# Performance work log

Measured on AMD Instinct MI355X. Metric: run time of the kernel, lower is better.

The kernel has to match this reference:

```python
import jax, jax.numpy as jnp
import numpy as np

N = 100000   # nodes
E = 1600000  # edges per relation
R = 3        # relations
F = 128      # feature_size
H = 64       # hid_dim
O = 32       # out_dim
B = 50000    # batch_nodes
EPS = 1e-5


def setup_inputs() -> dict:
    key = jax.random.key(0)
    ks = jax.random.split(key, 14)
    inp = {
        "features": jax.random.normal(ks[0], (N, F), jnp.float32),
        "edge_index": jax.random.randint(ks[1], (R, 2, E), 0, N),
        "batch_nodes": jax.random.randint(ks[2], (B,), 0, N),
        # per-relation conv1 / conv2 weights
        "W1": jax.random.normal(ks[3], (R, F, H), jnp.float32) / np.sqrt(F),
        "b1": jnp.zeros((R, H), jnp.float32),
        "W2": jax.random.normal(ks[4], (R, H, O), jnp.float32) / np.sqrt(H),
        "b2": jnp.zeros((R, O), jnp.float32),
        # learnable gamma (init 0.5) per conv per relation
        "gamma1": jnp.full((R,), 0.5, jnp.float32),
        "gamma2": jnp.full((R,), 0.5, jnp.float32),
        # batchnorm affine params per relation
        "bn1_scale": jnp.ones((R, H), jnp.float32),
        "bn1_bias": jnp.zeros((R, H), jnp.float32),
        "bn2_scale": jnp.ones((R, O), jnp.float32),
        "bn2_bias": jnp.zeros((R, O), jnp.float32),
    }
    return inp


def _pfgcn_conv(x, W, b, src, dst, gamma):
    # linear transform then symmetric-normalized gather/scatter aggregation,
    # mixed with self features via learnable gamma
    h = x @ W + b                                        # [N, C]
    deg = jax.ops.segment_sum(jnp.ones((src.shape[0],), h.dtype), dst, num_segments=N)
    dinv = jax.lax.rsqrt(jnp.maximum(deg, 1.0))          # [N]
    norm = dinv[src] * dinv[dst]                         # [E]
    agg = jax.ops.segment_sum(h[src] * norm[:, None], dst, num_segments=N)
    return gamma * agg + (1.0 - gamma) * h


def _batchnorm(x, scale, bias):
    m = x.mean(axis=0)
    v = x.var(axis=0)
    return (x - m) * jax.lax.rsqrt(v + EPS) * scale + bias


def reference(features, edge_index, batch_nodes, W1, b1, W2, b2,
              gamma1, gamma2, bn1_scale, bn1_bias, bn2_scale, bn2_bias):
    embeds = []
    for r in range(R):  # small fixed relation count
        src, dst = edge_index[r, 0], edge_index[r, 1]
        x = _pfgcn_conv(features, W1[r], b1[r], src, dst, gamma1[r])
        x = jax.nn.relu(_batchnorm(x, bn1_scale[r], bn1_bias[r]))
        # dropout is identity in eval
        x = _pfgcn_conv(x, W2[r], b2[r], src, dst, gamma2[r])
        x = jax.nn.relu(_batchnorm(x, bn2_scale[r], bn2_bias[r]))
        embeds.append(jax.nn.log_softmax(x[batch_nodes], axis=1))  # [B, O]
    multi = jnp.stack(embeds, axis=1)          # [B, R, O]
    return multi.reshape(batch_nodes.shape[0], -1)  # [B, R*O]
```

## Files before the change

### kernel.cpp

```cpp
#include <hip/hip_runtime.h>
#include <hip/hip_fp16.h>
#include <math.h>

#define N_NODES 100000
#define N_PAD   100352
#define N_EDGES 1600000
#define N_REL   3
#define BN_EPS  1e-5f

#define BK    49
#define BSH   11
#define BMSK  2047
#define NBLK  250
#define EPB   6400


__global__ __launch_bounds__(256) void k_hist(const int* __restrict__ ei,
                                              int* __restrict__ offs,
                                              float* __restrict__ zeroRegion) {
    const int r = blockIdx.y;
    const int* dst = ei + (size_t)r * 2 * N_EDGES + N_EDGES;
    const int tid = threadIdx.x;
    if (blockIdx.x == 0 && r == 0) {
        for (int i = tid; i < N_REL * 192; i += 256) zeroRegion[i] = 0.0f;
    }
    __shared__ int hist[4][BK];
    for (int i = tid; i < 4 * BK; i += 256) (&hist[0][0])[i] = 0;
    __syncthreads();
    const int4* d4 = (const int4*)(dst + blockIdx.x * EPB);
    const int cpy = tid & 3;
    for (int i = tid; i < EPB / 4; i += 256) {
        int4 v = d4[i];
        atomicAdd(&hist[cpy][v.x >> BSH], 1);
        atomicAdd(&hist[cpy][v.y >> BSH], 1);
        atomicAdd(&hist[cpy][v.z >> BSH], 1);
        atomicAdd(&hist[cpy][v.w >> BSH], 1);
    }
    __syncthreads();
    if (tid < BK)
        offs[(size_t)r * BK * NBLK + tid * NBLK + blockIdx.x] =
            hist[0][tid] + hist[1][tid] + hist[2][tid] + hist[3][tid];
}

__global__ __launch_bounds__(1024) void k_histscan(int* __restrict__ offs) {
    const int r = blockIdx.x;
    int* o = offs + (size_t)r * BK * NBLK;
    constexpr int LEN = BK * NBLK;
    constexpr int PER = (LEN + 1023) / 1024;
    __shared__ int sh[1024];
    const int t = threadIdx.x;
    const int base = t * PER;
    int pre[PER];
    int lsum = 0;
    #pragma unroll
    for (int i = 0; i < PER; ++i) {
        int idx = base + i;
        int v = (idx < LEN) ? o[idx] : 0;
        pre[i] = lsum;
        lsum += v;
    }
    sh[t] = lsum;
    __syncthreads();
    for (int s = 1; s < 1024; s <<= 1) {
        int add = (t >= s) ? sh[t - s] : 0;
        __syncthreads();
        sh[t] += add;
        __syncthreads();
    }
    const int myoff = sh[t] - lsum;
    #pragma unroll
    for (int i = 0; i < PER; ++i) {
        int idx = base + i;
        if (idx < LEN) o[idx] = myoff + pre[i];
    }
}

__global__ __launch_bounds__(256) void k_bin(const int* __restrict__ ei,
                                             const int* __restrict__ offs,
                                             int* __restrict__ binned) {
    const int r = blockIdx.y;
    const int* src = ei + (size_t)r * 2 * N_EDGES;
    const int* dst = src + N_EDGES;
    int* bn = binned + (size_t)r * N_EDGES;
    const int tid = threadIdx.x;
    __shared__ int cur[BK];
    if (tid < BK)
        cur[tid] = offs[(size_t)r * BK * NBLK + tid * NBLK + blockIdx.x];
    __syncthreads();
    const int4* s4p = (const int4*)(src + blockIdx.x * EPB);
    const int4* d4p = (const int4*)(dst + blockIdx.x * EPB);
    for (int i = tid; i < EPB / 4; i += 256) {
        int4 s4 = s4p[i];
        int4 dd = d4p[i];
        int p0 = atomicAdd(&cur[dd.x >> BSH], 1);
        bn[p0] = s4.x | ((dd.x & BMSK) << 17);
        int p1 = atomicAdd(&cur[dd.y >> BSH], 1);
        bn[p1] = s4.y | ((dd.y & BMSK) << 17);
        int p2 = atomicAdd(&cur[dd.z >> BSH], 1);
        bn[p2] = s4.z | ((dd.z & BMSK) << 17);
        int p3 = atomicAdd(&cur[dd.w >> BSH], 1);
        bn[p3] = s4.w | ((dd.w & BMSK) << 17);
    }
}

__global__ __launch_bounds__(1024) void k_csr2(const int* __restrict__ binned,
                                               const int* __restrict__ offs,
                                               int* __restrict__ rowptr,
                                               float* __restrict__ dinvB,
                                               float* __restrict__ rdinvB,
                                               int* __restrict__ edsrc) {
    const int r = blockIdx.y;
    const int b = blockIdx.x;
    const int t = threadIdx.x;
    const int bbase = b << BSH;
    const int* o = offs + (size_t)r * BK * NBLK;
    const int start = o[b * NBLK];
    const int end = (b == BK - 1) ? N_EDGES : o[(b + 1) * NBLK];
    const int* bn = binned + (size_t)r * N_EDGES;
    int* ed = edsrc + (size_t)r * N_EDGES;
    int* rp = rowptr + (size_t)r * (N_PAD + 1);
    float* dinv  = dinvB  + (size_t)r * N_PAD;
    float* rdinv = rdinvB + (size_t)r * N_PAD;

    __shared__ int cnt[1 << BSH];
    __shared__ int ssum[1024];
    cnt[t] = 0;
    cnt[t + 1024] = 0;
    __syncthreads();
    for (int i = start + t; i < end; i += 1024)
        atomicAdd(&cnt[bn[i] >> 17], 1);
    __syncthreads();
    const int a0 = cnt[2 * t];
    const int a1 = cnt[2 * t + 1];
    const int lsum = a0 + a1;
    ssum[t] = lsum;
    __syncthreads();
    for (int s = 1; s < 1024; s <<= 1) {
        int add = (t >= s) ? ssum[t - s] : 0;
        __syncthreads();
        ssum[t] += add;
        __syncthreads();
    }
    const int ex = ssum[t] - lsum;
    const int p0 = start + ex;
    const int p1 = p0 + a0;
    const int n0g = bbase + 2 * t;
    if (n0g < N_NODES) {
        rp[n0g] = p0;
        float m = fmaxf((float)a0, 1.0f);
        float dv = rsqrtf(m);
        dinv[n0g] = dv;
        rdinv[n0g] = m * dv;
    }
    if (n0g + 1 < N_NODES) {
        rp[n0g + 1] = p1;
        float m = fmaxf((float)a1, 1.0f);
        float dv = rsqrtf(m);
        dinv[n0g + 1] = dv;
        rdinv[n0g + 1] = m * dv;
    }
    if (b == BK - 1 && t == 0) rp[N_NODES] = N_EDGES;
    cnt[2 * t] = p0;
    cnt[2 * t + 1] = p1;
    __syncthreads();
    for (int i = start + t; i < end; i += 1024) {
        int p = bn[i];
        int pos = atomicAdd(&cnt[p >> 17], 1);
        ed[pos] = p & 0x1FFFF;
    }
}

__device__ __forceinline__ float ld_f(const float* p)  { return *p; }
__device__ __forceinline__ float ld_f(const __half* p) { return __half2float(*p); }

template<int K, int C, bool BN, typename TI>
__global__ __launch_bounds__(256) void k_gemm(const TI* __restrict__ Xb,
                                              size_t xStrideR,
                                              const float* __restrict__ Wb,
                                              const float* __restrict__ biasB,
                                              const float* __restrict__ bnsumB,
                                              const float* __restrict__ bnsqB,
                                              const float* __restrict__ bnScaleB,
                                              const float* __restrict__ bnBiasB,
                                              const float* __restrict__ dinvB,
                                              __half* __restrict__ Yb,
                                              int nodesPerBlock) {
    const int r = blockIdx.y;
    const TI* X = Xb + (size_t)r * xStrideR;
    const float* W = Wb + (size_t)r * K * C;
    const float* bias = biasB + (size_t)r * C;
    const float* dinv = dinvB + (size_t)r * N_PAD;
    __half* Y = Yb + (size_t)r * N_NODES * C;

    constexpr int CG = C / 4;
    constexpr int NPASS = 256 / CG;
    constexpr int XP = K + 1;
    __shared__ __align__(16) float Ws[K * C];
    __shared__ float Xs[NPASS * XP];
    __shared__ float seL[K], beL[K];
    const int tid = threadIdx.x;
    for (int i = tid; i < K * C; i += 256) Ws[i] = W[i];
    if (BN) {
        for (int i = tid; i < K; i += 256) {
            int gi = r * K + i;
            float m = bnsumB[gi] * (1.0f / N_NODES);
            float v = bnsqB[gi] * (1.0f / N_NODES) - m * m;
            float inv = rsqrtf(v + BN_EPS);
            float sc = inv * bnScaleB[gi];
            seL[i] = sc;
            beL[i] = bnBiasB[gi] - m * sc;
        }
    }
    const int cg = tid % CG;
    const int ln = tid / CG;
    const int c0 = cg * 4;
    const float4 bv = *(const float4*)&bias[c0];
    const int blockStart = blockIdx.x * nodesPerBlock;
    const int passes = nodesPerBlock / NPASS;
    for (int p = 0; p < passes; ++p) {
        const int node0 = blockStart + p * NPASS;
        __syncthreads();
        for (int i = tid; i < NPASS * K; i += 256) {
            int lnn = i / K, k = i % K;
            int n = node0 + lnn;
            float v = 0.0f;
            if (n < N_NODES) {
                v = ld_f(&X[(size_t)n * K + k]);
                if (BN) v = fmaxf(v * seL[k] + beL[k], 0.0f);
            }
            Xs[lnn * XP + k] = v;
        }
        __syncthreads();
        const int n = node0 + ln;
        float4 acc = bv;
        const float* xrow = &Xs[ln * XP];
        #pragma unroll 8
        for (int k = 0; k < K; ++k) {
            float f = xrow[k];
            float4 w = *(const float4*)&Ws[k * C + c0];
            acc.x += f * w.x;
            acc.y += f * w.y;
            acc.z += f * w.z;
            acc.w += f * w.w;
        }
        if (n < N_NODES) {
            const float dv = dinv[n];
            ushort4 sv;
            sv.x = __half_as_ushort(__float2half_rn(acc.x * dv));
            sv.y = __half_as_ushort(__float2half_rn(acc.y * dv));
            sv.z = __half_as_ushort(__float2half_rn(acc.z * dv));
            sv.w = __half_as_ushort(__float2half_rn(acc.w * dv));
            *(ushort4*)&Y[(size_t)n * C + c0] = sv;
        }
    }
}

template<int C, int NPB, typename TO>
__global__ __launch_bounds__(256) void k_gather(const __half* __restrict__ hB,
                                                const int* __restrict__ rowptrB,
                                                const int* __restrict__ edsB,
                                                const float* __restrict__ dinvB,
                                                const float* __restrict__ rdinvB,
                                                const float* __restrict__ gammaP,
                                                TO* __restrict__ XB,
                                                float* __restrict__ bnsumB,
                                                float* __restrict__ bnsqB) {
    const int r = blockIdx.y;
    const __half* h = hB + (size_t)r * N_NODES * C;
    const int* rowptr = rowptrB + (size_t)r * (N_PAD + 1);
    const int* edg = edsB + (size_t)r * N_EDGES;
    const float* dinv  = dinvB  + (size_t)r * N_PAD;
    const float* rdinv = rdinvB + (size_t)r * N_PAD;
    TO* X = XB + (size_t)r * N_NODES * C;
    float* bnsum = bnsumB + (size_t)r * C;
    float* bnsq  = bnsqB  + (size_t)r * C;

    constexpr int WPB = 256 / C;
    constexpr int RPS = NPB / WPB;
    constexpr int CH  = 4096;
    __shared__ int eds[CH];
    __shared__ int rp[NPB + 1];
    __shared__ float red[256];
    const int tid = threadIdx.x;
    const int c = tid % C;
    const int slot = tid / C;
    const float g = gammaP[r];
    const float gi = 1.0f - g;
    const int n0 = blockIdx.x * NPB;
    const __half* hc = h + c;
    if (tid <= NPB) {
        int n = n0 + tid;
        rp[tid] = rowptr[(n <= N_NODES) ? n : N_NODES];
    }
    __syncthreads();
    const int bs = rp[0];
    const int bEnd = rp[NPB];
    int rs[RPS], re[RPS];
    float acc[RPS];
    #pragma unroll
    for (int i = 0; i < RPS; ++i) {
        int ri = slot + i * WPB;
        rs[i] = rp[ri];
        re[i] = rp[ri + 1];
        acc[i] = 0.0f;
    }
    for (int ck = bs; ck < bEnd; ck += CH) {
        const int c1 = min(ck + CH, bEnd);
        const int cnt = c1 - ck;
        __syncthreads();
        for (int j = tid; j < cnt; j += 256) eds[j] = edg[ck + j];
        __syncthreads();
        #pragma unroll
        for (int i = 0; i < RPS; ++i) {
            const int lo = max(rs[i], ck);
            const int hi = min(re[i], c1);
            if (lo >= hi) continue;
            float a = acc[i];
            int e = lo;
            const int efull = lo + ((hi - lo) & ~7);
            for (; e < efull; e += 8) {
                int ed[8];
                #pragma unroll
                for (int j = 0; j < 8; ++j) ed[j] = eds[e - ck + j];
                float v[8];
                #pragma unroll
                for (int j = 0; j < 8; ++j)
                    v[j] = __half2float(hc[(unsigned)ed[j] * C]);
                #pragma unroll
                for (int j = 0; j < 8; ++j) a += v[j];
            }
            if (e < hi) {
                int ed[8];
                #pragma unroll
                for (int j = 0; j < 8; ++j) {
                    int t = e + j;
                    ed[j] = eds[((t < hi) ? t : lo) - ck];
                }
                float v[8];
                #pragma unroll
                for (int j = 0; j < 8; ++j)
                    v[j] = __half2float(hc[(unsigned)ed[j] * C]);
                #pragma unroll
                for (int j = 0; j < 8; ++j)
                    a += (e + j < hi) ? v[j] : 0.0f;
            }
            acc[i] = a;
        }
    }
    float s = 0.0f, sq = 0.0f;
    #pragma unroll
    for (int i = 0; i < RPS; ++i) {
        int n = n0 + slot + i * WPB;
        if (n < N_NODES) {
            float x = g * dinv[n] * acc[i]
                    + gi * rdinv[n] * __half2float(hc[(unsigned)n * C]);
            if constexpr (sizeof(TO) == 2)
                X[(size_t)n * C + c] = __float2half_rn(x);
            else
                X[(size_t)n * C + c] = x;
            s += x;
            sq += x * x;
        }
    }
    __syncthreads();
    red[tid] = s;
    __syncthreads();
    if (slot == 0) {
        float t = 0.0f;
        #pragma unroll
        for (int i = 0; i < WPB; ++i) t += red[c + i * C];
        atomicAdd(&bnsum[c], t);
    }
    __syncthreads();
    red[tid] = sq;
    __syncthreads();
    if (slot == 0) {
        float t = 0.0f;
        #pragma unroll
        for (int i = 0; i < WPB; ++i) t += red[c + i * C];
        atomicAdd(&bnsq[c], t);
    }
}

__global__ __launch_bounds__(256) void k_out(const float* __restrict__ x2B,
                                             const int* __restrict__ batch,
                                             const float* __restrict__ bnsumB,
                                             const float* __restrict__ bnsqB,
                                             const float* __restrict__ scaleB,
                                             const float* __restrict__ biasB,
                                             float* __restrict__ out) {
    const int r = blockIdx.y;
    const float* x2 = x2B + (size_t)r * N_NODES * 32;
    __shared__ float seL[32], beL[32];
    if (threadIdx.x < 32) {
        int gi = r * 32 + threadIdx.x;
        float m = bnsumB[gi] * (1.0f / N_NODES);
        float v = bnsqB[gi] * (1.0f / N_NODES) - m * m;
        float inv = rsqrtf(v + BN_EPS);
        float sc = inv * scaleB[gi];
        seL[threadIdx.x] = sc;
        beL[threadIdx.x] = biasB[gi] - m * sc;
    }
    __syncthreads();
    int gid = blockIdx.x * 256 + threadIdx.x;
    int b = gid >> 5;
    int c = gid & 31;
    if (b < 50000) {
        int node = batch[b];
        float y = fmaxf(x2[(size_t)node * 32 + c] * seL[c] + beL[c], 0.0f);
        float m = y;
        #pragma unroll
        for (int off = 16; off; off >>= 1) m = fmaxf(m, __shfl_xor(m, off, 32));
        float ex = __expf(y - m);
        float ssum = ex;
        #pragma unroll
        for (int off = 16; off; off >>= 1) ssum += __shfl_xor(ssum, off, 32);
        out[(size_t)b * (N_REL * 32) + r * 32 + c] = (y - m) - __logf(ssum);
    }
}

extern "C" void kernel_launch(void* const* d_in, const int* in_sizes, int n_in,
                              void* d_out, int out_size, void* d_ws, size_t ws_size,
                              hipStream_t stream) {
    const float* features    = (const float*)d_in[0];
    const int*   edge_index  = (const int*)d_in[1];
    const int*   batch_nodes = (const int*)d_in[2];
    const float* W1          = (const float*)d_in[3];
    const float* b1          = (const float*)d_in[4];
    const float* W2          = (const float*)d_in[5];
    const float* b2          = (const float*)d_in[6];
    const float* gamma1      = (const float*)d_in[7];
    const float* gamma2      = (const float*)d_in[8];
    const float* bn1_scale   = (const float*)d_in[9];
    const float* bn1_bias    = (const float*)d_in[10];
    const float* bn2_scale   = (const float*)d_in[11];
    const float* bn2_bias    = (const float*)d_in[12];
    float* out = (float*)d_out;

    char* wsB = (char*)d_ws;
    size_t off = 0;
    auto alloc = [&](size_t bytes) {
        void* p = wsB + off;
        off = (off + bytes + 15) & ~(size_t)15;
        return p;
    };
    float* bnsum1 = (float*)alloc(N_REL * 64 * 4);
    float* bnsq1  = (float*)alloc(N_REL * 64 * 4);
    float* bnsum2 = (float*)alloc(N_REL * 32 * 4);
    float* bnsq2  = (float*)alloc(N_REL * 32 * 4);
    float* zeroRegion = bnsum1;
    float* dinv      = (float*)alloc((size_t)N_REL * N_PAD * 4);
    float* rdinv     = (float*)alloc((size_t)N_REL * N_PAD * 4);
    int*   rowptr    = (int*)alloc((size_t)N_REL * (N_PAD + 1) * 4);
    int*   offs      = (int*)alloc((size_t)N_REL * BK * NBLK * 4);
    int*    edsrc = (int*)alloc((size_t)N_REL * N_EDGES * 4);
    __half* h1   = (__half*)alloc((size_t)N_REL * N_NODES * 64 * 2);
    __half* x1   = (__half*)alloc((size_t)N_REL * N_NODES * 64 * 2);
    __half* h2   = (__half*)alloc((size_t)N_REL * N_NODES * 32 * 2);
    float*  x2   = (float*)h1;
    int*  binned = (int*)x1;

    k_hist<<<dim3(NBLK, N_REL), 256, 0, stream>>>(edge_index, offs, zeroRegion);
    k_histscan<<<N_REL, 1024, 0, stream>>>(offs);
    k_bin<<<dim3(NBLK, N_REL), 256, 0, stream>>>(edge_index, offs, binned);
    k_csr2<<<dim3(BK, N_REL), 1024, 0, stream>>>(binned, offs, rowptr,
                                                 dinv, rdinv, edsrc);

    k_gemm<128, 64, false, float><<<dim3((N_NODES + 63) / 64, N_REL), 256, 0, stream>>>(
        features, 0, W1, b1, nullptr, nullptr, nullptr, nullptr, dinv, h1, 64);
    k_gather<64, 32, __half><<<dim3((N_NODES + 31) / 32, N_REL), 256, 0, stream>>>(
        h1, rowptr, edsrc, dinv, rdinv, gamma1, x1, bnsum1, bnsq1);

    k_gemm<64, 32, true, __half><<<dim3((N_NODES + 127) / 128, N_REL), 256, 0, stream>>>(
        x1, (size_t)N_NODES * 64, W2, b2, bnsum1, bnsq1, bn1_scale, bn1_bias,
        dinv, h2, 128);
    k_gather<32, 64, float><<<dim3((N_NODES + 63) / 64, N_REL), 256, 0, stream>>>(
        h2, rowptr, edsrc, dinv, rdinv, gamma2, x2, bnsum2, bnsq2);

    k_out<<<dim3((50000 * 32 + 255) / 256, N_REL), 256, 0, stream>>>(
        x2, batch_nodes, bnsum2, bnsq2, bn2_scale, bn2_bias, out);
}
```

Baseline: 781.1 us.

## Rewrite CSR gather as warp-per-row with vectorized loads and XCD-aware block mapping

The gather kernel now gives each 64-lane wavefront one destination row at a time. Lanes split into groups that each load four half channels per edge (8-byte vector loads), and edge indices are broadcast by shuffle instead of staged in a shared-memory chunk. Partial sums are reduced across groups with xor shuffles. Blocks are remapped so consecutive work groups of the same relation land on the same XCD, for L2 locality. The shared-memory edge staging and per-channel scalar half loads go away, at the cost of shuffle reductions and possible idle lanes on low-degree rows.

```diff
diff --git a/kernel.cpp b/kernel.cpp
--- a/kernel.cpp
+++ b/kernel.cpp
@@ -255,6 +255,14 @@
     }
 }
 
+__device__ __forceinline__ void acc4(float a[4], uint2 v) {
+    __half2 q0 = *reinterpret_cast<const __half2*>(&v.x);
+    __half2 q1 = *reinterpret_cast<const __half2*>(&v.y);
+    float2 f0 = __half22float2(q0);
+    float2 f1 = __half22float2(q1);
+    a[0] += f0.x; a[1] += f0.y; a[2] += f1.x; a[3] += f1.y;
+}
+
 template<int C, int NPB, typename TO>
 __global__ __launch_bounds__(256) void k_gather(const __half* __restrict__ hB,
                                                 const int* __restrict__ rowptrB,
@@ -264,8 +272,21 @@
                                                 const float* __restrict__ gammaP,
                                                 TO* __restrict__ XB,
                                                 float* __restrict__ bnsumB,
-                                                float* __restrict__ bnsqB) {
-    const int r = blockIdx.y;
+                                                float* __restrict__ bnsqB,
+                                                int nbr) {
+    constexpr int CPL = 4;
+    constexpr int LPR = C / CPL;
+    constexpr int G   = 64 / LPR;
+    constexpr int RPW = NPB / 4;
+
+    const int W = N_REL * nbr;
+    const int q = W >> 3, rem = W & 7;
+    const int xcd = (int)blockIdx.x & 7;
+    const int jj  = (int)blockIdx.x >> 3;
+    const int wg = (xcd < rem ? xcd * (q + 1) : rem * (q + 1) + (xcd - rem) * q) + jj;
+    const int r  = wg / nbr;
+    const int nb = wg - r * nbr;
+
     const __half* h = hB + (size_t)r * N_NODES * C;
     const int* rowptr = rowptrB + (size_t)r * (N_PAD + 1);
     const int* edg = edsB + (size_t)r * N_EDGES;
@@ -275,111 +296,114 @@
     float* bnsum = bnsumB + (size_t)r * C;
     float* bnsq  = bnsqB  + (size_t)r * C;
 
-    constexpr int WPB = 256 / C;
-    constexpr int RPS = NPB / WPB;
-    constexpr int CH  = 4096;
-    __shared__ int eds[CH];
     __shared__ int rp[NPB + 1];
-    __shared__ float red[256];
+    __shared__ float red[4][C];
+
     const int tid = threadIdx.x;
-    const int c = tid % C;
-    const int slot = tid / C;
-    const float g = gammaP[r];
-    const float gi = 1.0f - g;
-    const int n0 = blockIdx.x * NPB;
-    const __half* hc = h + c;
+    const int lane = tid & 63;
+    const int w = tid >> 6;
+    const int g = lane / LPR;
+    const int i = lane % LPR;
+    const float gm = gammaP[r];
+    const float giv = 1.0f - gm;
+    const int n0 = nb * NPB;
+
     if (tid <= NPB) {
         int n = n0 + tid;
         rp[tid] = rowptr[(n <= N_NODES) ? n : N_NODES];
     }
     __syncthreads();
-    const int bs = rp[0];
-    const int bEnd = rp[NPB];
-    int rs[RPS], re[RPS];
-    float acc[RPS];
-    #pragma unroll
-    for (int i = 0; i < RPS; ++i) {
-        int ri = slot + i * WPB;
-        rs[i] = rp[ri];
-        re[i] = rp[ri + 1];
-        acc[i] = 0.0f;
-    }
-    for (int ck = bs; ck < bEnd; ck += CH) {
-        const int c1 = min(ck + CH, bEnd);
-        const int cnt = c1 - ck;
-        __syncthreads();
-        for (int j = tid; j < cnt; j += 256) eds[j] = edg[ck + j];
-        __syncthreads();
+
+    float sA[CPL] = {0.f, 0.f, 0.f, 0.f};
+    float sqA[CPL] = {0.f, 0.f, 0.f, 0.f};
+
+    #define GSTEP(SS) { \
+        const int e_ = __shfl(er, (SS) * G + g); \
+        const uint2 v_ = *reinterpret_cast<const uint2*>(h + (size_t)(unsigned)e_ * C + i * CPL); \
+        acc4(a, v_); }
+
+    for (int lr = 0; lr < RPW; ++lr) {
+        const int row = w * RPW + lr;
+        const int lo = rp[row], hi = rp[row + 1];
+        float a[CPL] = {0.f, 0.f, 0.f, 0.f};
+        for (int base = lo; base < hi; base += 64) {
+            const int cnt = min(64, hi - base);
+            const int er = edg[base + ((lane < cnt) ? lane : 0)];
+            const int nfull = cnt / G;
+            int s = 0;
+            for (; s + 4 <= nfull; s += 4) {
+                GSTEP(s) GSTEP(s + 1) GSTEP(s + 2) GSTEP(s + 3)
+            }
+            for (; s + 2 <= nfull; s += 2) {
+                GSTEP(s) GSTEP(s + 1)
+            }
+            for (; s < nfull; ++s) {
+                GSTEP(s)
+            }
+            const int tr = cnt - nfull * G;
+            if (tr) {
+                const int eT = __shfl(er, nfull * G + ((g < tr) ? g : 0));
+                if (g < tr) {
+                    const uint2 v_ = *reinterpret_cast<const uint2*>(
+                        h + (size_t)(unsigned)eT * C + i * CPL);
+                    acc4(a, v_);
+                }
+            }
+        }
         #pragma unroll
-        for (int i = 0; i < RPS; ++i) {
-            const int lo = max(rs[i], ck);
-            const int hi = min(re[i], c1);
-            if (lo >= hi) continue;
-            float a = acc[i];
-            int e = lo;
-            const int efull = lo + ((hi - lo) & ~7);
-            for (; e < efull; e += 8) {
-                int ed[8];
-                #pragma unroll
-                for (int j = 0; j < 8; ++j) ed[j] = eds[e - ck + j];
-                float v[8];
-                #pragma unroll
-                for (int j = 0; j < 8; ++j)
-                    v[j] = __half2float(hc[(unsigned)ed[j] * C]);
-                #pragma unroll
-                for (int j = 0; j < 8; ++j) a += v[j];
+        for (int st = LPR; st < 64; st <<= 1) {
+            #pragma unroll
+            for (int j = 0; j < CPL; ++j) a[j] += __shfl_xor(a[j], st);
+        }
+        const int n = n0 + row;
+        if (n < N_NODES) {
+            const float dv  = gm  * dinv[n];
+            const float rdv = giv * rdinv[n];
+            const uint2 sv = *reinterpret_cast<const uint2*>(h + (size_t)n * C + i * CPL);
+            __half2 q0 = *reinterpret_cast<const __half2*>(&sv.x);
+            __half2 q1 = *reinterpret_cast<const __half2*>(&sv.y);
+            float2 f0 = __half22float2(q0);
+            float2 f1 = __half22float2(q1);
+            float x0 = dv * a[0] + rdv * f0.x;
+            float x1 = dv * a[1] + rdv * f0.y;
+            float x2 = dv * a[2] + rdv * f1.x;
+            float x3 = dv * a[3] + rdv * f1.y;
+            if (g == 0) {
+                if constexpr (sizeof(TO) == 2) {
+                    __half2 p0 = __floats2half2_rn(x0, x1);
+                    __half2 p1 = __floats2half2_rn(x2, x3);
+                    union { __half2 hh; unsigned u; } c0, c1;
+                    c0.hh = p0; c1.hh = p1;
+                    uint2 ov; ov.x = c0.u; ov.y = c1.u;
+                    *reinterpret_cast<uint2*>(&X[(size_t)n * C + i * CPL]) = ov;
+                } else {
+                    float4 ov = make_float4(x0, x1, x2, x3);
+                    *reinterpret_cast<float4*>(&X[(size_t)n * C + i * CPL]) = ov;
+                }
             }
-            if (e < hi) {
-                int ed[8];
-                #pragma unroll
-                for (int j = 0; j < 8; ++j) {
-                    int t = e + j;
-                    ed[j] = eds[((t < hi) ? t : lo) - ck];
-                }
-                float v[8];
-                #pragma unroll
-                for (int j = 0; j < 8; ++j)
-                    v[j] = __half2float(hc[(unsigned)ed[j] * C]);
-                #pragma unroll
-                for (int j = 0; j < 8; ++j)
-                    a += (e + j < hi) ? v[j] : 0.0f;
-            }
-            acc[i] = a;
-        }
-    }
-    float s = 0.0f, sq = 0.0f;
-    #pragma unroll
-    for (int i = 0; i < RPS; ++i) {
-        int n = n0 + slot + i * WPB;
-        if (n < N_NODES) {
-            float x = g * dinv[n] * acc[i]
-                    + gi * rdinv[n] * __half2float(hc[(unsigned)n * C]);
-            if constexpr (sizeof(TO) == 2)
-                X[(size_t)n * C + c] = __float2half_rn(x);
-            else
-                X[(size_t)n * C + c] = x;
-            s += x;
-            sq += x * x;
-        }
-    }
-    __syncthreads();
-    red[tid] = s;
-    __syncthreads();
-    if (slot == 0) {
-        float t = 0.0f;
+            sA[0] += x0; sqA[0] += x0 * x0;
+            sA[1] += x1; sqA[1] += x1 * x1;
+            sA[2] += x2; sqA[2] += x2 * x2;
+            sA[3] += x3; sqA[3] += x3 * x3;
+        }
+    }
+    #undef GSTEP
+
+    if (g == 0) {
         #pragma unroll
-        for (int i = 0; i < WPB; ++i) t += red[c + i * C];
-        atomicAdd(&bnsum[c], t);
-    }
-    __syncthreads();
-    red[tid] = sq;
-    __syncthreads();
-    if (slot == 0) {
-        float t = 0.0f;
+        for (int j = 0; j < CPL; ++j) red[w][i * CPL + j] = sA[j];
+    }
+    __syncthreads();
+    if (tid < C)
+        atomicAdd(&bnsum[tid], red[0][tid] + red[1][tid] + red[2][tid] + red[3][tid]);
+    __syncthreads();
+    if (g == 0) {
         #pragma unroll
-        for (int i = 0; i < WPB; ++i) t += red[c + i * C];
-        atomicAdd(&bnsq[c], t);
-    }
+        for (int j = 0; j < CPL; ++j) red[w][i * CPL + j] = sqA[j];
+    }
+    __syncthreads();
+    if (tid < C)
+        atomicAdd(&bnsq[tid], red[0][tid] + red[1][tid] + red[2][tid] + red[3][tid]);
 }
 
 __global__ __launch_bounds__(256) void k_out(const float* __restrict__ x2B,
@@ -466,16 +490,18 @@
     k_csr2<<<dim3(BK, N_REL), 1024, 0, stream>>>(binned, offs, rowptr,
                                                  dinv, rdinv, edsrc);
 
+    constexpr int GNB = (N_NODES + 63) / 64;
+
     k_gemm<128, 64, false, float><<<dim3((N_NODES + 63) / 64, N_REL), 256, 0, stream>>>(
         features, 0, W1, b1, nullptr, nullptr, nullptr, nullptr, dinv, h1, 64);
-    k_gather<64, 32, __half><<<dim3((N_NODES + 31) / 32, N_REL), 256, 0, stream>>>(
-        h1, rowptr, edsrc, dinv, rdinv, gamma1, x1, bnsum1, bnsq1);
+    k_gather<64, 64, __half><<<dim3(N_REL * GNB), 256, 0, stream>>>(
+        h1, rowptr, edsrc, dinv, rdinv, gamma1, x1, bnsum1, bnsq1, GNB);
 
     k_gemm<64, 32, true, __half><<<dim3((N_NODES + 127) / 128, N_REL), 256, 0, stream>>>(
         x1, (size_t)N_NODES * 64, W2, b2, bnsum1, bnsq1, bn1_scale, bn1_bias,
         dinv, h2, 128);
-    k_gather<32, 64, float><<<dim3((N_NODES + 63) / 64, N_REL), 256, 0, stream>>>(
-        h2, rowptr, edsrc, dinv, rdinv, gamma2, x2, bnsum2, bnsq2);
+    k_gather<32, 64, float><<<dim3(N_REL * GNB), 256, 0, stream>>>(
+        h2, rowptr, edsrc, dinv, rdinv, gamma2, x2, bnsum2, bnsq2, GNB);
 
     k_out<<<dim3((50000 * 32 + 255) / 256, N_REL), 256, 0, stream>>>(
         x2, batch_nodes, bnsum2, bnsq2, bn2_scale, bn2_bias, out);
```

Measured after the change: 733.3 us. -6.1%, faster.
